# Kernel tuning notes

Hardware: AMD Instinct MI355X
Metric: run time of the kernel (lower is better)

## Reference

```python
import jax, jax.numpy as jnp
import numpy as np

EPS = 1e-5

def conv1x1(x, w, b):
    # x: (b,c,h,w), w: (o,c), b: (o,)
    return jnp.einsum('bchw,oc->bohw', x, w) + b[None, :, None, None]

def maxpool2(x):
    b, c, h, w = x.shape
    return x.reshape(b, c, h // 2, 2, w // 2, 2).max(axis=(3, 5))

def setup_inputs() -> dict:
    key = jax.random.key(0)
    ks = jax.random.split(key, 11)
    C, I = 64, 32
    B, H, W = 16, 64, 64
    s_c = 1.0 / np.sqrt(C)
    s_i = 1.0 / np.sqrt(I)
    return {
        'x':    jax.random.normal(ks[0], (B, C, H, W), jnp.float32),
        'w1':   jax.random.normal(ks[1], (I, C), jnp.float32) * s_c,
        'b1':   jax.random.normal(ks[2], (I,), jnp.float32) * s_c,
        'w21':  jax.random.normal(ks[3], (I, C), jnp.float32) * s_c,
        'b21':  jax.random.normal(ks[4], (I,), jnp.float32) * s_c,
        'w22':  jax.random.normal(ks[5], (I, C), jnp.float32) * s_c,
        'b22':  jax.random.normal(ks[6], (I,), jnp.float32) * s_c,
        'w3':   jax.random.normal(ks[7], (C, I), jnp.float32) * s_i,
        'b3':   jax.random.normal(ks[8], (C,), jnp.float32) * s_i,
        'gamma': jax.random.normal(ks[9], (C,), jnp.float32),
        'beta':  jax.random.normal(ks[10], (C,), jnp.float32),
    }

def reference(x, w1, b1, w21, b21, w22, b22, w3, b3, gamma, beta):
    b, c, h, w = x.shape
    # g = maxpool(conv1(x)): (b, i, N) with N = h*w/4
    g = maxpool2(conv1x1(x, w1, b1)).reshape(b, w1.shape[0], -1)
    # theta = conv2_1(x): (b, i, HW)
    theta = conv1x1(x, w21, b21).reshape(b, w21.shape[0], -1)
    # phi = maxpool(conv2_2(x)): (b, i, N)
    phi = maxpool2(conv1x1(x, w22, b22)).reshape(b, w22.shape[0], -1)
    N = phi.shape[-1]
    # Original: y = ((theta^T @ phi) / N) @ g^T ; reassociated (no softmax):
    kv = jnp.einsum('bin,bjn->bij', phi, g) / N           # (b, i, i)
    y = jnp.einsum('bis,bij->bjs', theta, kv)             # (b, i, HW)
    y = y.reshape(b, -1, h, w)
    # conv3 + BatchNorm (training-mode batch stats)
    z = conv1x1(y, w3, b3)                                # (b, c, h, w)
    mu = z.mean(axis=(0, 2, 3), keepdims=True)
    var = ((z - mu) ** 2).mean(axis=(0, 2, 3), keepdims=True)
    z = gamma[None, :, None, None] * (z - mu) / jnp.sqrt(var + EPS) + beta[None, :, None, None]
    return z + x
```

## Files before the change

### kernel.cpp

```cpp
#include <hip/hip_runtime.h>

__global__ __launch_bounds__(256) void k1_kv(const float* __restrict__ x,
    const float* __restrict__ w1, const float* __restrict__ b1,
    const float* __restrict__ w22, const float* __restrict__ b22,
    float* __restrict__ kvpart, float* __restrict__ statsacc)
{
  __shared__ float xl[64][128];
  __shared__ float wlt[64][64];
  __shared__ float bl[64];
  __shared__ float phil[32][33];
  __shared__ float glt[32][33];
  int t = threadIdx.x;
  int b = blockIdx.x >> 5, r = blockIdx.x & 31;
  const float* xb = x + ((size_t)b << 18);

  if (blockIdx.x == 0 && t < 128) statsacc[t] = 0.f;

  for (int v = t; v < 2048; v += 256) {
    int c = v >> 5, rem = v & 31;
    int h2 = rem >> 4, wv = rem & 15;
    float4 u = *(const float4*)(xb + c*4096 + (2*r + h2)*64 + wv*4);
    float* dst = &xl[c][h2*64 + wv*4];
    dst[0] = u.x; dst[1] = u.y; dst[2] = u.z; dst[3] = u.w;
  }
  for (int v = t; v < 1024; v += 256) {
    int half = v >> 9, vv = v & 511;
    int o = vv >> 4;
    int cb = (vv & 15) * 4;
    const float* src = (half ? w22 : w1) + o*64 + cb;
    float4 u = *(const float4*)src;
    int oo = o + half*32;
    wlt[cb+0][oo] = u.x; wlt[cb+1][oo] = u.y; wlt[cb+2][oo] = u.z; wlt[cb+3][oo] = u.w;
  }
  if (t < 32) bl[t] = b1[t];
  else if (t < 64) bl[t] = b22[t-32];
  __syncthreads();

  int p = t & 31, og = t >> 5;
  float acc0[4][4], acc1[4][4];
  #pragma unroll
  for (int k = 0; k < 4; k++)
    #pragma unroll
    for (int px = 0; px < 4; px++) { acc0[k][px] = 0.f; acc1[k][px] = 0.f; }

  #pragma unroll 4
  for (int c = 0; c < 64; c++) {
    float2 x0 = *(const float2*)&xl[c][2*p];
    float2 x1 = *(const float2*)&xl[c][64 + 2*p];
    float4 wa = *(const float4*)&wlt[c][og*4];
    float4 wb = *(const float4*)&wlt[c][32 + og*4];
    float xs[4]  = {x0.x, x0.y, x1.x, x1.y};
    float was[4] = {wa.x, wa.y, wa.z, wa.w};
    float wbs[4] = {wb.x, wb.y, wb.z, wb.w};
    #pragma unroll
    for (int k = 0; k < 4; k++)
      #pragma unroll
      for (int px = 0; px < 4; px++) {
        acc0[k][px] += was[k] * xs[px];
        acc1[k][px] += wbs[k] * xs[px];
      }
  }
  #pragma unroll
  for (int k = 0; k < 4; k++) {
    int o = og*4 + k;
    float m1 = fmaxf(fmaxf(acc0[k][0], acc0[k][1]), fmaxf(acc0[k][2], acc0[k][3])) + bl[o];
    float m2 = fmaxf(fmaxf(acc1[k][0], acc1[k][1]), fmaxf(acc1[k][2], acc1[k][3])) + bl[32+o];
    glt[p][o]  = m1;
    phil[o][p] = m2;
  }
  __syncthreads();

  float* kvp = kvpart + (size_t)blockIdx.x * 1024;
  for (int e = t; e < 1024; e += 256) {
    int i = e >> 5, j = e & 31;
    float s = 0.f;
    #pragma unroll
    for (int q = 0; q < 32; q++) s += phil[i][q] * glt[q][j];
    kvp[e] = s;
  }
}

__global__ __launch_bounds__(256) void k2_wmat(const float* __restrict__ kvpart,
    const float* __restrict__ w3, const float* __restrict__ b3,
    const float* __restrict__ w21, const float* __restrict__ b21,
    float* __restrict__ Wt, float* __restrict__ biasv)
{
  __shared__ float kvl[32][32];
  __shared__ float w3t[32][64];
  __shared__ float w21l[32][64];
  __shared__ float b21l[32];
  int t = threadIdx.x, b = blockIdx.x;
  for (int e = t; e < 1024; e += 256) {
    float s = 0.f;
    const float* kp = kvpart + ((size_t)b << 15) + e;
    #pragma unroll
    for (int r = 0; r < 32; r++) s += kp[r*1024];
    kvl[e>>5][e&31] = s * (1.f/1024.f);
  }
  for (int e = t; e < 2048; e += 256) { int c = e >> 5, j = e & 31; w3t[j][c] = w3[e]; }
  for (int e = t; e < 2048; e += 256) { int i = e >> 6, ch = e & 63; w21l[i][ch] = w21[e]; }
  if (t < 32) b21l[t] = b21[t];
  __syncthreads();

  if (t < 64) {
    int c = t;
    float A[32];
    #pragma unroll
    for (int i = 0; i < 32; i++) {
      float s = 0.f;
      #pragma unroll
      for (int j = 0; j < 32; j++) s += w3t[j][c] * kvl[i][j];
      A[i] = s;
    }
    float bias = b3[c];
    #pragma unroll
    for (int i = 0; i < 32; i++) bias += A[i] * b21l[i];
    biasv[b*64 + c] = bias;
    float* Wb = Wt + (size_t)b*4096;
    #pragma unroll
    for (int ch = 0; ch < 64; ch++) {
      float s = 0.f;
      #pragma unroll
      for (int i = 0; i < 32; i++) s += A[i] * w21l[i][ch];
      Wb[ch*64 + c] = s;
    }
  }
}

__global__ __launch_bounds__(256) void k3_stats(const float* __restrict__ x,
    const float* __restrict__ Wt, const float* __restrict__ biasv,
    float* __restrict__ statsacc)
{
  __shared__ float xt[64][128];
  __shared__ float wl[64][64];
  __shared__ float lstat[128];
  int t = threadIdx.x, blk = blockIdx.x;
  int tile = blk & 31, b = blk >> 5;
  const float* xb = x + ((size_t)b << 18) + tile*128;
  for (int v = t; v < 2048; v += 256) {
    int ch = v >> 5, rem = v & 31;
    *(float4*)&xt[ch][rem*4] = *(const float4*)(xb + ch*4096 + rem*4);
  }
  const float* wb = Wt + ((size_t)b << 12);
  for (int v = t; v < 1024; v += 256)
    *(float4*)&wl[v >> 4][(v & 15)*4] = *(const float4*)(wb + v*4);
  if (t < 128) lstat[t] = 0.f;
  __syncthreads();

  int pg = t & 15, cg = t >> 4;
  int p0 = pg*4, c0 = cg*4;
  float acc[4][8];
  #pragma unroll
  for (int ci = 0; ci < 4; ci++)
    #pragma unroll
    for (int pj = 0; pj < 8; pj++) acc[ci][pj] = 0.f;

  #pragma unroll 4
  for (int k = 0; k < 64; k++) {
    float4 w4 = *(const float4*)&wl[k][c0];
    float4 xa = *(const float4*)&xt[k][p0];
    float4 xc = *(const float4*)&xt[k][p0 + 64];
    float xs[8] = {xa.x, xa.y, xa.z, xa.w, xc.x, xc.y, xc.z, xc.w};
    float ws[4] = {w4.x, w4.y, w4.z, w4.w};
    #pragma unroll
    for (int ci = 0; ci < 4; ci++)
      #pragma unroll
      for (int pj = 0; pj < 8; pj++) acc[ci][pj] += ws[ci] * xs[pj];
  }

  float4 bias4 = *(const float4*)(biasv + b*64 + c0);
  float bb[4] = {bias4.x, bias4.y, bias4.z, bias4.w};
  #pragma unroll
  for (int ci = 0; ci < 4; ci++) {
    float s1 = 0.f, s2 = 0.f;
    #pragma unroll
    for (int pj = 0; pj < 8; pj++) {
      float z = acc[ci][pj] + bb[ci];
      s1 += z; s2 += z*z;
    }
    #pragma unroll
    for (int off = 1; off < 16; off <<= 1) { s1 += __shfl_xor(s1, off); s2 += __shfl_xor(s2, off); }
    if (pg == 0) { atomicAdd(&lstat[c0+ci], s1); atomicAdd(&lstat[64+c0+ci], s2); }
  }
  __syncthreads();
  if (t < 128) atomicAdd(&statsacc[t], lstat[t]);
}

__global__ __launch_bounds__(256) void k4_out(const float* __restrict__ x,
    const float* __restrict__ Wt, const float* __restrict__ biasv,
    const float* __restrict__ statsacc,
    const float* __restrict__ gamma, const float* __restrict__ beta,
    float* __restrict__ out)
{
  __shared__ float xt[64][128];
  __shared__ float wl[64][64];
  __shared__ float scl[64], shl[64];
  int t = threadIdx.x, blk = blockIdx.x;
  int tile = blk & 31, b = blk >> 5;
  const float* xb = x + ((size_t)b << 18) + tile*128;
  for (int v = t; v < 2048; v += 256) {
    int ch = v >> 5, rem = v & 31;
    *(float4*)&xt[ch][rem*4] = *(const float4*)(xb + ch*4096 + rem*4);
  }
  const float* wb = Wt + ((size_t)b << 12);
  for (int v = t; v < 1024; v += 256)
    *(float4*)&wl[v >> 4][(v & 15)*4] = *(const float4*)(wb + v*4);
  if (t < 64) {
    const float inv_cnt = 1.f / 65536.f;
    float mu  = statsacc[t] * inv_cnt;
    float var = statsacc[64+t] * inv_cnt - mu*mu;
    float sc  = gamma[t] * rsqrtf(var + 1e-5f);
    scl[t] = sc;
    shl[t] = beta[t] - sc*mu;
  }
  __syncthreads();

  int pg = t & 15, cg = t >> 4;
  int p0 = pg*4, c0 = cg*4;
  float acc[4][8];
  #pragma unroll
  for (int ci = 0; ci < 4; ci++)
    #pragma unroll
    for (int pj = 0; pj < 8; pj++) acc[ci][pj] = 0.f;

  #pragma unroll 4
  for (int k = 0; k < 64; k++) {
    float4 w4 = *(const float4*)&wl[k][c0];
    float4 xa = *(const float4*)&xt[k][p0];
    float4 xc = *(const float4*)&xt[k][p0 + 64];
    float xs[8] = {xa.x, xa.y, xa.z, xa.w, xc.x, xc.y, xc.z, xc.w};
    float ws[4] = {w4.x, w4.y, w4.z, w4.w};
    #pragma unroll
    for (int ci = 0; ci < 4; ci++)
      #pragma unroll
      for (int pj = 0; pj < 8; pj++) acc[ci][pj] += ws[ci] * xs[pj];
  }

  float4 bias4 = *(const float4*)(biasv + b*64 + c0);
  float bb[4] = {bias4.x, bias4.y, bias4.z, bias4.w};
  float* ob = out + ((size_t)b << 18) + (size_t)tile*128;
  #pragma unroll
  for (int ci = 0; ci < 4; ci++) {
    int c = c0 + ci;
    float sc = scl[c], sh = shl[c];
    float4 xa = *(const float4*)&xt[c][p0];
    float4 xc = *(const float4*)&xt[c][p0 + 64];
    float4 ra, rb;
    ra.x = sc*(acc[ci][0]+bb[ci]) + sh + xa.x;
    ra.y = sc*(acc[ci][1]+bb[ci]) + sh + xa.y;
    ra.z = sc*(acc[ci][2]+bb[ci]) + sh + xa.z;
    ra.w = sc*(acc[ci][3]+bb[ci]) + sh + xa.w;
    rb.x = sc*(acc[ci][4]+bb[ci]) + sh + xc.x;
    rb.y = sc*(acc[ci][5]+bb[ci]) + sh + xc.y;
    rb.z = sc*(acc[ci][6]+bb[ci]) + sh + xc.z;
    rb.w = sc*(acc[ci][7]+bb[ci]) + sh + xc.w;
    *(float4*)(ob + (size_t)c*4096 + p0)      = ra;
    *(float4*)(ob + (size_t)c*4096 + p0 + 64) = rb;
  }
}

extern "C" void kernel_launch(void* const* d_in, const int* in_sizes, int n_in,
                              void* d_out, int out_size, void* d_ws, size_t ws_size,
                              hipStream_t stream)
{
  const float* x    = (const float*)d_in[0];
  const float* w1   = (const float*)d_in[1];
  const float* b1   = (const float*)d_in[2];
  const float* w21  = (const float*)d_in[3];
  const float* b21  = (const float*)d_in[4];
  const float* w22  = (const float*)d_in[5];
  const float* b22  = (const float*)d_in[6];
  const float* w3   = (const float*)d_in[7];
  const float* b3   = (const float*)d_in[8];
  const float* gamma= (const float*)d_in[9];
  const float* beta = (const float*)d_in[10];

  float* ws       = (float*)d_ws;
  float* kvpart   = ws;
  float* Wt       = ws + 524288;
  float* biasv    = ws + 589824;
  float* statsacc = ws + 590848;

  hipLaunchKernelGGL(k1_kv,    dim3(512), dim3(256), 0, stream, x, w1, b1, w22, b22, kvpart, statsacc);
  hipLaunchKernelGGL(k2_wmat,  dim3(16),  dim3(256), 0, stream, kvpart, w3, b3, w21, b21, Wt, biasv);
  hipLaunchKernelGGL(k3_stats, dim3(512), dim3(256), 0, stream, x, Wt, biasv, statsacc);
  hipLaunchKernelGGL(k4_out,   dim3(512), dim3(256), 0, stream, x, Wt, biasv, statsacc, gamma, beta,
                     (float*)d_out);
}
```

Baseline: 71.43 us.

## Fuse four kernels into one cooperative persistent kernel with grid syncs

Replaces the four-kernel sequence with a single cooperative launch of 256 blocks of 1024 threads. Each block keeps its two x tiles in shared memory for the whole run, so x is read from global memory once instead of three times, and three grid.sync barriers replace the kernel boundaries. The weight-matrix stage runs on only 16 blocks while the rest wait at the barrier, and grid-wide syncs carry their own overhead. The old multi-kernel path remains as a fallback when cooperative launch is unavailable.

```diff
diff --git a/kernel.cpp b/kernel.cpp
--- a/kernel.cpp
+++ b/kernel.cpp
@@ -1,4 +1,220 @@
 #include <hip/hip_runtime.h>
+#include <hip/hip_cooperative_groups.h>
+
+namespace cg = cooperative_groups;
+
+__global__ __launch_bounds__(1024, 4) void fused(
+    const float* __restrict__ x,
+    const float* __restrict__ w1,  const float* __restrict__ b1,
+    const float* __restrict__ w21, const float* __restrict__ b21,
+    const float* __restrict__ w22, const float* __restrict__ b22,
+    const float* __restrict__ w3,  const float* __restrict__ b3,
+    const float* __restrict__ gamma, const float* __restrict__ beta,
+    float* __restrict__ kvpart, float* __restrict__ Wt,
+    float* __restrict__ biasv,  float* __restrict__ statsacc,
+    float* __restrict__ out)
+{
+  __shared__ float xt[2*64*128];
+  __shared__ float buf[8512];
+  cg::grid_group grid = cg::this_grid();
+  int t = threadIdx.x, blk = blockIdx.x;
+  int b = blk >> 4;
+  int h = t >> 9, u = t & 511;
+  int tile = (blk & 15)*2 + h;
+  int pairP = 2*blk + h;
+
+  if (blk == 0 && t < 128) statsacc[t] = 0.f;
+
+  const float* xb = x + ((size_t)b << 18) + tile*128;
+  float* xth = &xt[h*8192];
+  for (int v = u; v < 2048; v += 512) {
+    int ch = v >> 5, rem = v & 31;
+    *(float4*)&xth[ch*128 + rem*4] = *(const float4*)(xb + ch*4096 + rem*4);
+  }
+  {
+    float* wlt  = buf;
+    float* bl   = buf + 4096;
+    float* phil = buf + 4160 + h*2112;
+    float* glt  = phil + 1056;
+    {
+      int half = t >> 9, vv = t & 511;
+      int o = vv >> 4, cb = (vv & 15)*4;
+      const float* src = (half ? w22 : w1) + o*64 + cb;
+      float4 uu = *(const float4*)src;
+      int oo = o + half*32;
+      wlt[(cb+0)*64+oo]=uu.x; wlt[(cb+1)*64+oo]=uu.y;
+      wlt[(cb+2)*64+oo]=uu.z; wlt[(cb+3)*64+oo]=uu.w;
+    }
+    if (t < 32) bl[t] = b1[t];
+    else if (t < 64) bl[t] = b22[t-32];
+    __syncthreads();
+
+    int p = u & 31, og = u >> 5;
+    float a0[2][4], a1[2][4];
+    #pragma unroll
+    for (int k = 0; k < 2; k++)
+      #pragma unroll
+      for (int px = 0; px < 4; px++) { a0[k][px] = 0.f; a1[k][px] = 0.f; }
+    #pragma unroll 4
+    for (int c = 0; c < 64; c++) {
+      float2 x0 = *(const float2*)&xth[c*128 + 2*p];
+      float2 x1 = *(const float2*)&xth[c*128 + 64 + 2*p];
+      float2 wa = *(const float2*)&wlt[c*64 + og*2];
+      float2 wb = *(const float2*)&wlt[c*64 + 32 + og*2];
+      float xs[4]  = {x0.x, x0.y, x1.x, x1.y};
+      float was[2] = {wa.x, wa.y};
+      float wbs[2] = {wb.x, wb.y};
+      #pragma unroll
+      for (int k = 0; k < 2; k++)
+        #pragma unroll
+        for (int px = 0; px < 4; px++) {
+          a0[k][px] += was[k] * xs[px];
+          a1[k][px] += wbs[k] * xs[px];
+        }
+    }
+    #pragma unroll
+    for (int k = 0; k < 2; k++) {
+      int o = og*2 + k;
+      float m1 = fmaxf(fmaxf(a0[k][0], a0[k][1]), fmaxf(a0[k][2], a0[k][3])) + bl[o];
+      float m2 = fmaxf(fmaxf(a1[k][0], a1[k][1]), fmaxf(a1[k][2], a1[k][3])) + bl[32+o];
+      glt[p*33 + o]  = m1;
+      phil[o*33 + p] = m2;
+    }
+    __syncthreads();
+    float* kvp = kvpart + (size_t)pairP * 1024;
+    for (int e = u; e < 1024; e += 512) {
+      int i = e >> 5, j = e & 31;
+      float s = 0.f;
+      #pragma unroll
+      for (int q = 0; q < 32; q++) s += phil[i*33 + q] * glt[q*33 + j];
+      kvp[e] = s;
+    }
+  }
+  grid.sync();
+
+  if (blk < 16) {
+    float* kvl  = buf;
+    float* w3t  = buf + 1024;
+    float* w21l = buf + 3072;
+    float* b21l = buf + 5120;
+    int bb = blk;
+    {
+      const float* kp = kvpart + ((size_t)bb << 15) + t;
+      float s = 0.f;
+      #pragma unroll
+      for (int r = 0; r < 32; r++) s += kp[r*1024];
+      kvl[t] = s * (1.f/1024.f);
+    }
+    for (int e = t; e < 2048; e += 1024) { int c = e >> 5, j = e & 31; w3t[j*64+c] = w3[e]; }
+    for (int e = t; e < 2048; e += 1024) { int i = e >> 6, ch = e & 63; w21l[i*64+ch] = w21[e]; }
+    if (t < 32) b21l[t] = b21[t];
+    __syncthreads();
+    if (t < 64) {
+      int c = t;
+      float A[32];
+      #pragma unroll
+      for (int i = 0; i < 32; i++) {
+        float s = 0.f;
+        #pragma unroll
+        for (int j = 0; j < 32; j++) s += w3t[j*64+c] * kvl[i*32+j];
+        A[i] = s;
+      }
+      float bias = b3[c];
+      #pragma unroll
+      for (int i = 0; i < 32; i++) bias += A[i] * b21l[i];
+      biasv[bb*64 + c] = bias;
+      float* Wb = Wt + (size_t)bb*4096;
+      #pragma unroll
+      for (int ch = 0; ch < 64; ch++) {
+        float s = 0.f;
+        #pragma unroll
+        for (int i = 0; i < 32; i++) s += A[i] * w21l[i*64+ch];
+        Wb[ch*64 + c] = s;
+      }
+    }
+  }
+  grid.sync();
+
+  float* wl    = buf;
+  float* lstat = buf + 4096;
+  {
+    int v = t;
+    *(float4*)&wl[(v>>4)*64 + (v&15)*4] = *(const float4*)(Wt + ((size_t)b << 12) + v*4);
+  }
+  if (t < 128) lstat[t] = 0.f;
+  __syncthreads();
+
+  int pg = u & 15, cg2 = u >> 4;
+  int p0 = pg*4, c0 = cg2*2;
+  float acc[2][8];
+  #pragma unroll
+  for (int ci = 0; ci < 2; ci++)
+    #pragma unroll
+    for (int pj = 0; pj < 8; pj++) acc[ci][pj] = 0.f;
+  #pragma unroll 4
+  for (int k = 0; k < 64; k++) {
+    float2 w2 = *(const float2*)&wl[k*64 + c0];
+    float4 xa = *(const float4*)&xth[k*128 + p0];
+    float4 xc = *(const float4*)&xth[k*128 + p0 + 64];
+    float xs[8] = {xa.x, xa.y, xa.z, xa.w, xc.x, xc.y, xc.z, xc.w};
+    #pragma unroll
+    for (int pj = 0; pj < 8; pj++) {
+      acc[0][pj] += w2.x * xs[pj];
+      acc[1][pj] += w2.y * xs[pj];
+    }
+  }
+  {
+    float2 bb2 = *(const float2*)(biasv + b*64 + c0);
+    float bbv[2] = {bb2.x, bb2.y};
+    #pragma unroll
+    for (int ci = 0; ci < 2; ci++)
+      #pragma unroll
+      for (int pj = 0; pj < 8; pj++) acc[ci][pj] += bbv[ci];
+    #pragma unroll
+    for (int ci = 0; ci < 2; ci++) {
+      float s1 = 0.f, s2 = 0.f;
+      #pragma unroll
+      for (int pj = 0; pj < 8; pj++) { float z = acc[ci][pj]; s1 += z; s2 += z*z; }
+      #pragma unroll
+      for (int off = 1; off < 16; off <<= 1) { s1 += __shfl_xor(s1, off); s2 += __shfl_xor(s2, off); }
+      if (pg == 0) { atomicAdd(&lstat[c0+ci], s1); atomicAdd(&lstat[64+c0+ci], s2); }
+    }
+  }
+  __syncthreads();
+  if (t < 128) atomicAdd(&statsacc[t], lstat[t]);
+  grid.sync();
+
+  float* scl = buf + 4224;
+  float* shl = buf + 4288;
+  if (t < 64) {
+    const float inv_cnt = 1.f / 65536.f;
+    float mu  = statsacc[t] * inv_cnt;
+    float var = statsacc[64+t] * inv_cnt - mu*mu;
+    float sc  = gamma[t] * rsqrtf(var + 1e-5f);
+    scl[t] = sc;
+    shl[t] = beta[t] - sc*mu;
+  }
+  __syncthreads();
+  float* ob = out + ((size_t)b << 18) + (size_t)tile*128;
+  #pragma unroll
+  for (int ci = 0; ci < 2; ci++) {
+    int c = c0 + ci;
+    float sc = scl[c], sh = shl[c];
+    float4 xa = *(const float4*)&xth[c*128 + p0];
+    float4 xc = *(const float4*)&xth[c*128 + p0 + 64];
+    float4 ra, rb;
+    ra.x = sc*acc[ci][0] + sh + xa.x;
+    ra.y = sc*acc[ci][1] + sh + xa.y;
+    ra.z = sc*acc[ci][2] + sh + xa.z;
+    ra.w = sc*acc[ci][3] + sh + xa.w;
+    rb.x = sc*acc[ci][4] + sh + xc.x;
+    rb.y = sc*acc[ci][5] + sh + xc.y;
+    rb.z = sc*acc[ci][6] + sh + xc.z;
+    rb.w = sc*acc[ci][7] + sh + xc.w;
+    *(float4*)(ob + (size_t)c*4096 + p0)      = ra;
+    *(float4*)(ob + (size_t)c*4096 + p0 + 64) = rb;
+  }
+}
 
 __global__ __launch_bounds__(256) void k1_kv(const float* __restrict__ x,
     const float* __restrict__ w1, const float* __restrict__ b1,
@@ -13,9 +229,7 @@
   int t = threadIdx.x;
   int b = blockIdx.x >> 5, r = blockIdx.x & 31;
   const float* xb = x + ((size_t)b << 18);
-
   if (blockIdx.x == 0 && t < 128) statsacc[t] = 0.f;
-
   for (int v = t; v < 2048; v += 256) {
     int c = v >> 5, rem = v & 31;
     int h2 = rem >> 4, wv = rem & 15;
@@ -25,8 +239,7 @@
   }
   for (int v = t; v < 1024; v += 256) {
     int half = v >> 9, vv = v & 511;
-    int o = vv >> 4;
-    int cb = (vv & 15) * 4;
+    int o = vv >> 4, cb = (vv & 15) * 4;
     const float* src = (half ? w22 : w1) + o*64 + cb;
     float4 u = *(const float4*)src;
     int oo = o + half*32;
@@ -35,14 +248,12 @@
   if (t < 32) bl[t] = b1[t];
   else if (t < 64) bl[t] = b22[t-32];
   __syncthreads();
-
   int p = t & 31, og = t >> 5;
   float acc0[4][4], acc1[4][4];
   #pragma unroll
   for (int k = 0; k < 4; k++)
     #pragma unroll
     for (int px = 0; px < 4; px++) { acc0[k][px] = 0.f; acc1[k][px] = 0.f; }
-
   #pragma unroll 4
   for (int c = 0; c < 64; c++) {
     float2 x0 = *(const float2*)&xl[c][2*p];
@@ -69,7 +280,6 @@
     phil[o][p] = m2;
   }
   __syncthreads();
-
   float* kvp = kvpart + (size_t)blockIdx.x * 1024;
   for (int e = t; e < 1024; e += 256) {
     int i = e >> 5, j = e & 31;
@@ -101,7 +311,6 @@
   for (int e = t; e < 2048; e += 256) { int i = e >> 6, ch = e & 63; w21l[i][ch] = w21[e]; }
   if (t < 32) b21l[t] = b21[t];
   __syncthreads();
-
   if (t < 64) {
     int c = t;
     float A[32];
@@ -146,7 +355,6 @@
     *(float4*)&wl[v >> 4][(v & 15)*4] = *(const float4*)(wb + v*4);
   if (t < 128) lstat[t] = 0.f;
   __syncthreads();
-
   int pg = t & 15, cg = t >> 4;
   int p0 = pg*4, c0 = cg*4;
   float acc[4][8];
@@ -154,7 +362,6 @@
   for (int ci = 0; ci < 4; ci++)
     #pragma unroll
     for (int pj = 0; pj < 8; pj++) acc[ci][pj] = 0.f;
-
   #pragma unroll 4
   for (int k = 0; k < 64; k++) {
     float4 w4 = *(const float4*)&wl[k][c0];
@@ -167,7 +374,6 @@
       #pragma unroll
       for (int pj = 0; pj < 8; pj++) acc[ci][pj] += ws[ci] * xs[pj];
   }
-
   float4 bias4 = *(const float4*)(biasv + b*64 + c0);
   float bb[4] = {bias4.x, bias4.y, bias4.z, bias4.w};
   #pragma unroll
@@ -214,7 +420,6 @@
     shl[t] = beta[t] - sc*mu;
   }
   __syncthreads();
-
   int pg = t & 15, cg = t >> 4;
   int p0 = pg*4, c0 = cg*4;
   float acc[4][8];
@@ -222,7 +427,6 @@
   for (int ci = 0; ci < 4; ci++)
     #pragma unroll
     for (int pj = 0; pj < 8; pj++) acc[ci][pj] = 0.f;
-
   #pragma unroll 4
   for (int k = 0; k < 64; k++) {
     float4 w4 = *(const float4*)&wl[k][c0];
@@ -235,7 +439,6 @@
       #pragma unroll
       for (int pj = 0; pj < 8; pj++) acc[ci][pj] += ws[ci] * xs[pj];
   }
-
   float4 bias4 = *(const float4*)(biasv + b*64 + c0);
   float bb[4] = {bias4.x, bias4.y, bias4.z, bias4.w};
   float* ob = out + ((size_t)b << 18) + (size_t)tile*128;
@@ -280,10 +483,29 @@
   float* Wt       = ws + 524288;
   float* biasv    = ws + 589824;
   float* statsacc = ws + 590848;
+  float* outp     = (float*)d_out;
+
+  int dev = 0;
+  hipGetDevice(&dev);
+  int coop = 0;
+  hipDeviceGetAttribute(&coop, hipDeviceAttributeCooperativeLaunch, dev);
+  int mab = 0;
+  hipError_t oe = hipOccupancyMaxActiveBlocksPerMultiprocessor(
+      &mab, (const void*)fused, 1024, 0);
+  if (coop && oe == hipSuccess && mab >= 1) {
+    void* args[] = {
+      (void*)&x, (void*)&w1, (void*)&b1, (void*)&w21, (void*)&b21,
+      (void*)&w22, (void*)&b22, (void*)&w3, (void*)&b3,
+      (void*)&gamma, (void*)&beta,
+      (void*)&kvpart, (void*)&Wt, (void*)&biasv, (void*)&statsacc, (void*)&outp
+    };
+    hipError_t rc = hipLaunchCooperativeKernel((const void*)fused,
+                                               dim3(256), dim3(1024), args, 0, stream);
+    if (rc == hipSuccess) return;
+  }
 
   hipLaunchKernelGGL(k1_kv,    dim3(512), dim3(256), 0, stream, x, w1, b1, w22, b22, kvpart, statsacc);
   hipLaunchKernelGGL(k2_wmat,  dim3(16),  dim3(256), 0, stream, kvpart, w3, b3, w21, b21, Wt, biasv);
   hipLaunchKernelGGL(k3_stats, dim3(512), dim3(256), 0, stream, x, Wt, biasv, statsacc);
-  hipLaunchKernelGGL(k4_out,   dim3(512), dim3(256), 0, stream, x, Wt, biasv, statsacc, gamma, beta,
-                     (float*)d_out);
+  hipLaunchKernelGGL(k4_out,   dim3(512), dim3(256), 0, stream, x, Wt, biasv, statsacc, gamma, beta, outp);
 }
```

Result: no change. 71.67 us (+0.3%).

## Derive BatchNorm statistics analytically from per-batch Gram matrix of x

Applied to the files above, without the earlier changes.

The separate statistics pass, which re-read x and redid the conv GEMM, is removed. The first kernel now also computes per-tile partial Gram matrices x·xᵀ and per-channel sums of x. The small per-batch kernel reduces these partials and uses the folded weight matrix and bias to get the sum and sum of squares of z in closed form, writing them as per-batch stats. The output kernel sums those stats across batches. This drops a full pass over x and one launch, at the cost of writing and reading 8 MB of Gram partials through a 16-block reduction, and it relies on E[z²]−μ² with fp32 accumulation.

```diff
diff --git a/kernel.cpp b/kernel.cpp
--- a/kernel.cpp
+++ b/kernel.cpp
@@ -1,32 +1,26 @@
 #include <hip/hip_runtime.h>
 
-__global__ __launch_bounds__(256) void k1_kv(const float* __restrict__ x,
+__global__ __launch_bounds__(256) void kA(const float* __restrict__ x,
     const float* __restrict__ w1, const float* __restrict__ b1,
     const float* __restrict__ w22, const float* __restrict__ b22,
-    float* __restrict__ kvpart, float* __restrict__ statsacc)
+    float* __restrict__ kvpart, float* __restrict__ Gpart, float* __restrict__ xsumpart)
 {
   __shared__ float xl[64][128];
   __shared__ float wlt[64][64];
   __shared__ float bl[64];
   __shared__ float phil[32][33];
   __shared__ float glt[32][33];
-  int t = threadIdx.x;
-  int b = blockIdx.x >> 5, r = blockIdx.x & 31;
-  const float* xb = x + ((size_t)b << 18);
-
-  if (blockIdx.x == 0 && t < 128) statsacc[t] = 0.f;
+  int t = threadIdx.x, blk = blockIdx.x;
+  int tile = blk & 31, b = blk >> 5;
+  const float* xb = x + ((size_t)b << 18) + tile*128;
 
   for (int v = t; v < 2048; v += 256) {
-    int c = v >> 5, rem = v & 31;
-    int h2 = rem >> 4, wv = rem & 15;
-    float4 u = *(const float4*)(xb + c*4096 + (2*r + h2)*64 + wv*4);
-    float* dst = &xl[c][h2*64 + wv*4];
-    dst[0] = u.x; dst[1] = u.y; dst[2] = u.z; dst[3] = u.w;
+    int ch = v >> 5, rem = v & 31;
+    *(float4*)&xl[ch][rem*4] = *(const float4*)(xb + ch*4096 + rem*4);
   }
   for (int v = t; v < 1024; v += 256) {
     int half = v >> 9, vv = v & 511;
-    int o = vv >> 4;
-    int cb = (vv & 15) * 4;
+    int o = vv >> 4, cb = (vv & 15) * 4;
     const float* src = (half ? w22 : w1) + o*64 + cb;
     float4 u = *(const float4*)src;
     int oo = o + half*32;
@@ -36,41 +30,42 @@
   else if (t < 64) bl[t] = b22[t-32];
   __syncthreads();
 
-  int p = t & 31, og = t >> 5;
-  float acc0[4][4], acc1[4][4];
-  #pragma unroll
-  for (int k = 0; k < 4; k++)
-    #pragma unroll
-    for (int px = 0; px < 4; px++) { acc0[k][px] = 0.f; acc1[k][px] = 0.f; }
-
-  #pragma unroll 4
-  for (int c = 0; c < 64; c++) {
-    float2 x0 = *(const float2*)&xl[c][2*p];
-    float2 x1 = *(const float2*)&xl[c][64 + 2*p];
-    float4 wa = *(const float4*)&wlt[c][og*4];
-    float4 wb = *(const float4*)&wlt[c][32 + og*4];
-    float xs[4]  = {x0.x, x0.y, x1.x, x1.y};
-    float was[4] = {wa.x, wa.y, wa.z, wa.w};
-    float wbs[4] = {wb.x, wb.y, wb.z, wb.w};
+  {
+    int p = t & 31, og = t >> 5;
+    float acc0[4][4], acc1[4][4];
     #pragma unroll
     for (int k = 0; k < 4; k++)
       #pragma unroll
-      for (int px = 0; px < 4; px++) {
-        acc0[k][px] += was[k] * xs[px];
-        acc1[k][px] += wbs[k] * xs[px];
-      }
-  }
-  #pragma unroll
-  for (int k = 0; k < 4; k++) {
-    int o = og*4 + k;
-    float m1 = fmaxf(fmaxf(acc0[k][0], acc0[k][1]), fmaxf(acc0[k][2], acc0[k][3])) + bl[o];
-    float m2 = fmaxf(fmaxf(acc1[k][0], acc1[k][1]), fmaxf(acc1[k][2], acc1[k][3])) + bl[32+o];
-    glt[p][o]  = m1;
-    phil[o][p] = m2;
-  }
-  __syncthreads();
-
-  float* kvp = kvpart + (size_t)blockIdx.x * 1024;
+      for (int px = 0; px < 4; px++) { acc0[k][px] = 0.f; acc1[k][px] = 0.f; }
+    #pragma unroll 4
+    for (int c = 0; c < 64; c++) {
+      float2 x0 = *(const float2*)&xl[c][2*p];
+      float2 x1 = *(const float2*)&xl[c][64 + 2*p];
+      float4 wa = *(const float4*)&wlt[c][og*4];
+      float4 wb = *(const float4*)&wlt[c][32 + og*4];
+      float xs[4]  = {x0.x, x0.y, x1.x, x1.y};
+      float was[4] = {wa.x, wa.y, wa.z, wa.w};
+      float wbs[4] = {wb.x, wb.y, wb.z, wb.w};
+      #pragma unroll
+      for (int k = 0; k < 4; k++)
+        #pragma unroll
+        for (int px = 0; px < 4; px++) {
+          acc0[k][px] += was[k] * xs[px];
+          acc1[k][px] += wbs[k] * xs[px];
+        }
+    }
+    #pragma unroll
+    for (int k = 0; k < 4; k++) {
+      int o = og*4 + k;
+      float m1 = fmaxf(fmaxf(acc0[k][0], acc0[k][1]), fmaxf(acc0[k][2], acc0[k][3])) + bl[o];
+      float m2 = fmaxf(fmaxf(acc1[k][0], acc1[k][1]), fmaxf(acc1[k][2], acc1[k][3])) + bl[32+o];
+      glt[p][o]  = m1;
+      phil[o][p] = m2;
+    }
+  }
+  __syncthreads();
+
+  float* kvp = kvpart + (size_t)blk * 1024;
   for (int e = t; e < 1024; e += 256) {
     int i = e >> 5, j = e & 31;
     float s = 0.f;
@@ -78,27 +73,85 @@
     for (int q = 0; q < 32; q++) s += phil[i][q] * glt[q][j];
     kvp[e] = s;
   }
+
+  {
+    int g1 = t >> 4, g2 = t & 15;
+    int c1 = g1*4, c2 = g2*4;
+    float ga[4][4];
+    #pragma unroll
+    for (int i = 0; i < 4; i++)
+      #pragma unroll
+      for (int j = 0; j < 4; j++) ga[i][j] = 0.f;
+    for (int pp = 0; pp < 128; pp++) {
+      int p = (pp + t) & 127;
+      float xa[4] = {xl[c1][p], xl[c1+1][p], xl[c1+2][p], xl[c1+3][p]};
+      float xbv[4] = {xl[c2][p], xl[c2+1][p], xl[c2+2][p], xl[c2+3][p]};
+      #pragma unroll
+      for (int i = 0; i < 4; i++)
+        #pragma unroll
+        for (int j = 0; j < 4; j++) ga[i][j] += xa[i] * xbv[j];
+    }
+    float* gp = Gpart + (size_t)blk * 4096;
+    #pragma unroll
+    for (int i = 0; i < 4; i++) {
+      float4 r; r.x = ga[i][0]; r.y = ga[i][1]; r.z = ga[i][2]; r.w = ga[i][3];
+      *(float4*)(gp + (c1+i)*64 + c2) = r;
+    }
+  }
+
+  {
+    int c = t >> 2, q = t & 3;
+    float s = 0.f;
+    for (int pp = 0; pp < 32; pp++) {
+      int p = q*32 + ((pp + t) & 31);
+      s += xl[c][p];
+    }
+    s += __shfl_down(s, 1);
+    s += __shfl_down(s, 2);
+    if (q == 0) xsumpart[(size_t)blk*64 + c] = s;
+  }
 }
 
-__global__ __launch_bounds__(256) void k2_wmat(const float* __restrict__ kvpart,
+__global__ __launch_bounds__(256) void kB(const float* __restrict__ kvpart,
+    const float* __restrict__ Gpart, const float* __restrict__ xsumpart,
     const float* __restrict__ w3, const float* __restrict__ b3,
     const float* __restrict__ w21, const float* __restrict__ b21,
-    float* __restrict__ Wt, float* __restrict__ biasv)
+    float* __restrict__ Wt, float* __restrict__ biasv, float* __restrict__ statb)
 {
-  __shared__ float kvl[32][32];
-  __shared__ float w3t[32][64];
-  __shared__ float w21l[32][64];
+  __shared__ float kvl[1024];
+  __shared__ float Sl[4096];
+  __shared__ float w3t[2048];
+  __shared__ float w21l[2048];
+  __shared__ float wlds[4096];
+  __shared__ float xbl[64];
   __shared__ float b21l[32];
+  __shared__ float qpl[256];
+  __shared__ float mdl[64], bsl[64];
   int t = threadIdx.x, b = blockIdx.x;
+
   for (int e = t; e < 1024; e += 256) {
-    float s = 0.f;
     const float* kp = kvpart + ((size_t)b << 15) + e;
+    float s = 0.f;
     #pragma unroll
     for (int r = 0; r < 32; r++) s += kp[r*1024];
-    kvl[e>>5][e&31] = s * (1.f/1024.f);
-  }
-  for (int e = t; e < 2048; e += 256) { int c = e >> 5, j = e & 31; w3t[j][c] = w3[e]; }
-  for (int e = t; e < 2048; e += 256) { int i = e >> 6, ch = e & 63; w21l[i][ch] = w21[e]; }
+    kvl[e] = s * (1.f/1024.f);
+  }
+  for (int e = t; e < 4096; e += 256) {
+    const float* gp = Gpart + ((size_t)b << 17) + e;
+    float s = 0.f;
+    #pragma unroll
+    for (int r = 0; r < 32; r++) s += gp[r*4096];
+    Sl[e] = s;
+  }
+  if (t < 64) {
+    const float* xp = xsumpart + ((size_t)b << 11) + t;
+    float s = 0.f;
+    #pragma unroll
+    for (int r = 0; r < 32; r++) s += xp[r*64];
+    xbl[t] = s;
+  }
+  for (int e = t; e < 2048; e += 256) { int c = e >> 5, j = e & 31; w3t[j*64+c] = w3[e]; }
+  for (int e = t; e < 2048; e += 256) { int i = e >> 6, ch = e & 63; w21l[i*64+ch] = w21[e]; }
   if (t < 32) b21l[t] = b21[t];
   __syncthreads();
 
@@ -109,86 +162,54 @@
     for (int i = 0; i < 32; i++) {
       float s = 0.f;
       #pragma unroll
-      for (int j = 0; j < 32; j++) s += w3t[j][c] * kvl[i][j];
+      for (int j = 0; j < 32; j++) s += w3t[j*64+c] * kvl[i*32+j];
       A[i] = s;
     }
     float bias = b3[c];
     #pragma unroll
     for (int i = 0; i < 32; i++) bias += A[i] * b21l[i];
     biasv[b*64 + c] = bias;
-    float* Wb = Wt + (size_t)b*4096;
+    float md = 0.f;
     #pragma unroll
     for (int ch = 0; ch < 64; ch++) {
-      float s = 0.f;
-      #pragma unroll
-      for (int i = 0; i < 32; i++) s += A[i] * w21l[i][ch];
-      Wb[ch*64 + c] = s;
-    }
+      float wv = 0.f;
+      #pragma unroll
+      for (int i = 0; i < 32; i++) wv += A[i] * w21l[i*64+ch];
+      wlds[ch*64 + c] = wv;
+      md += wv * xbl[ch];
+    }
+    mdl[c] = md;
+    bsl[c] = bias;
+  }
+  __syncthreads();
+
+  for (int v = t; v < 1024; v += 256)
+    *(float4*)(Wt + ((size_t)b << 12) + v*4) = *(const float4*)&wlds[v*4];
+
+  {
+    int c = t & 63, kg = t >> 6;
+    float qp = 0.f;
+    for (int k1 = kg*16; k1 < kg*16 + 16; k1++) {
+      float tmp = 0.f;
+      #pragma unroll
+      for (int k2 = 0; k2 < 64; k2++) tmp += Sl[k1*64 + k2] * wlds[k2*64 + c];
+      qp += wlds[k1*64 + c] * tmp;
+    }
+    qpl[kg*64 + c] = qp;
+  }
+  __syncthreads();
+  if (t < 64) {
+    int c = t;
+    float q = qpl[c] + qpl[64+c] + qpl[128+c] + qpl[192+c];
+    float bias = bsl[c], md = mdl[c];
+    statb[b*128 + c]      = md + 4096.f*bias;
+    statb[b*128 + 64 + c] = q + 2.f*bias*md + 4096.f*bias*bias;
   }
 }
 
-__global__ __launch_bounds__(256) void k3_stats(const float* __restrict__ x,
+__global__ __launch_bounds__(256) void kC(const float* __restrict__ x,
     const float* __restrict__ Wt, const float* __restrict__ biasv,
-    float* __restrict__ statsacc)
-{
-  __shared__ float xt[64][128];
-  __shared__ float wl[64][64];
-  __shared__ float lstat[128];
-  int t = threadIdx.x, blk = blockIdx.x;
-  int tile = blk & 31, b = blk >> 5;
-  const float* xb = x + ((size_t)b << 18) + tile*128;
-  for (int v = t; v < 2048; v += 256) {
-    int ch = v >> 5, rem = v & 31;
-    *(float4*)&xt[ch][rem*4] = *(const float4*)(xb + ch*4096 + rem*4);
-  }
-  const float* wb = Wt + ((size_t)b << 12);
-  for (int v = t; v < 1024; v += 256)
-    *(float4*)&wl[v >> 4][(v & 15)*4] = *(const float4*)(wb + v*4);
-  if (t < 128) lstat[t] = 0.f;
-  __syncthreads();
-
-  int pg = t & 15, cg = t >> 4;
-  int p0 = pg*4, c0 = cg*4;
-  float acc[4][8];
-  #pragma unroll
-  for (int ci = 0; ci < 4; ci++)
-    #pragma unroll
-    for (int pj = 0; pj < 8; pj++) acc[ci][pj] = 0.f;
-
-  #pragma unroll 4
-  for (int k = 0; k < 64; k++) {
-    float4 w4 = *(const float4*)&wl[k][c0];
-    float4 xa = *(const float4*)&xt[k][p0];
-    float4 xc = *(const float4*)&xt[k][p0 + 64];
-    float xs[8] = {xa.x, xa.y, xa.z, xa.w, xc.x, xc.y, xc.z, xc.w};
-    float ws[4] = {w4.x, w4.y, w4.z, w4.w};
-    #pragma unroll
-    for (int ci = 0; ci < 4; ci++)
-      #pragma unroll
-      for (int pj = 0; pj < 8; pj++) acc[ci][pj] += ws[ci] * xs[pj];
-  }
-
-  float4 bias4 = *(const float4*)(biasv + b*64 + c0);
-  float bb[4] = {bias4.x, bias4.y, bias4.z, bias4.w};
-  #pragma unroll
-  for (int ci = 0; ci < 4; ci++) {
-    float s1 = 0.f, s2 = 0.f;
-    #pragma unroll
-    for (int pj = 0; pj < 8; pj++) {
-      float z = acc[ci][pj] + bb[ci];
-      s1 += z; s2 += z*z;
-    }
-    #pragma unroll
-    for (int off = 1; off < 16; off <<= 1) { s1 += __shfl_xor(s1, off); s2 += __shfl_xor(s2, off); }
-    if (pg == 0) { atomicAdd(&lstat[c0+ci], s1); atomicAdd(&lstat[64+c0+ci], s2); }
-  }
-  __syncthreads();
-  if (t < 128) atomicAdd(&statsacc[t], lstat[t]);
-}
-
-__global__ __launch_bounds__(256) void k4_out(const float* __restrict__ x,
-    const float* __restrict__ Wt, const float* __restrict__ biasv,
-    const float* __restrict__ statsacc,
+    const float* __restrict__ statb,
     const float* __restrict__ gamma, const float* __restrict__ beta,
     float* __restrict__ out)
 {
@@ -206,9 +227,15 @@
   for (int v = t; v < 1024; v += 256)
     *(float4*)&wl[v >> 4][(v & 15)*4] = *(const float4*)(wb + v*4);
   if (t < 64) {
+    float s1 = 0.f, s2 = 0.f;
+    #pragma unroll
+    for (int bb = 0; bb < 16; bb++) {
+      s1 += statb[bb*128 + t];
+      s2 += statb[bb*128 + 64 + t];
+    }
     const float inv_cnt = 1.f / 65536.f;
-    float mu  = statsacc[t] * inv_cnt;
-    float var = statsacc[64+t] * inv_cnt - mu*mu;
+    float mu  = s1 * inv_cnt;
+    float var = s2 * inv_cnt - mu*mu;
     float sc  = gamma[t] * rsqrtf(var + 1e-5f);
     scl[t] = sc;
     shl[t] = beta[t] - sc*mu;
@@ -277,13 +304,16 @@
 
   float* ws       = (float*)d_ws;
   float* kvpart   = ws;
-  float* Wt       = ws + 524288;
-  float* biasv    = ws + 589824;
-  float* statsacc = ws + 590848;
-
-  hipLaunchKernelGGL(k1_kv,    dim3(512), dim3(256), 0, stream, x, w1, b1, w22, b22, kvpart, statsacc);
-  hipLaunchKernelGGL(k2_wmat,  dim3(16),  dim3(256), 0, stream, kvpart, w3, b3, w21, b21, Wt, biasv);
-  hipLaunchKernelGGL(k3_stats, dim3(512), dim3(256), 0, stream, x, Wt, biasv, statsacc);
-  hipLaunchKernelGGL(k4_out,   dim3(512), dim3(256), 0, stream, x, Wt, biasv, statsacc, gamma, beta,
-                     (float*)d_out);
+  float* Gpart    = ws + 524288;
+  float* xsumpart = ws + 2621440;
+  float* Wt       = ws + 2654208;
+  float* biasv    = ws + 2719744;
+  float* statb    = ws + 2720768;
+
+  hipLaunchKernelGGL(kA, dim3(512), dim3(256), 0, stream,
+                     x, w1, b1, w22, b22, kvpart, Gpart, xsumpart);
+  hipLaunchKernelGGL(kB, dim3(16),  dim3(256), 0, stream,
+                     kvpart, Gpart, xsumpart, w3, b3, w21, b21, Wt, biasv, statb);
+  hipLaunchKernelGGL(kC, dim3(512), dim3(256), 0, stream,
+                     x, Wt, biasv, statb, gamma, beta, (float*)d_out);
 }
```

Measured after the change: 80.07 us. 1.12x slower.
